# Performance work log

Measured on AMD Instinct MI355X. Metric: run time of the kernel, lower is better.

The kernel has to match this reference:

```python
import jax, jax.numpy as jnp
import numpy as np

B, T, H = 2048, 2048, 32  # batch, sequence steps (columns of input), hidden size


def setup_inputs() -> dict:
    key = jax.random.key(0)
    ks = jax.random.split(key, 5)
    stdv = 1.0 / np.sqrt(H)
    u = lambda k, shp: jax.random.uniform(k, shp, jnp.float32, -stdv, stdv)
    return {
        "x": jax.random.normal(ks[0], (B, T), jnp.float32),
        "weight_ih": u(ks[1], (4 * H, 1)),
        "weight_hh": u(ks[2], (4 * H, H)),
        "bias_ih": u(ks[3], (4 * H,)),
        "bias_hh": u(ks[4], (4 * H,)),
    }


def reference(x, weight_ih, weight_hh, bias_ih, bias_hh):
    Bn, Tn = x.shape
    Hn = weight_hh.shape[1]
    xs = x.T[:, :, None]              # (T, B, 1): step-major inputs
    bias = bias_ih + bias_hh          # (4H,)

    def step(carry, x_t):
        h, c = carry                  # (B, H) each
        gates = x_t @ weight_ih.T + h @ weight_hh.T + bias  # (B, 4H)
        i, f, g, o = jnp.split(gates, 4, axis=1)
        i = jax.nn.sigmoid(i)
        f = jax.nn.sigmoid(f)
        g = jnp.tanh(g)
        o = jax.nn.sigmoid(o)
        # row 0 of the original skips the forget term entirely; with c0 = 0,
        # f * c0 == 0, so this is identical math.
        c_new = f * c + i * g
        h_new = o * jnp.tanh(c_new)
        return (h_new, c_new), h_new

    h0 = jnp.zeros((Bn, Hn), x.dtype)
    c0 = jnp.zeros((Bn, Hn), x.dtype)
    _, ys = jax.lax.scan(step, (h0, c0), xs)   # ys: (T, B, H)
    # torch.cat(h_matrix, 1): step-major blocks of width H along dim 1
    return jnp.transpose(ys, (1, 0, 2)).reshape(Bn, Tn * Hn)
```

## Files before the change

### kernel.cpp

```cpp
#include <hip/hip_runtime.h>
#include <hip/hip_fp16.h>


#define Bsz 2048
#define Tsz 2048
#define Hsz 32

typedef _Float16 v2h __attribute__((ext_vector_type(2)));

__device__ __forceinline__ float fast_rcp(float x) { return __builtin_amdgcn_rcpf(x); }
__device__ __forceinline__ float fast_exp2(float x) { return __builtin_amdgcn_exp2f(x); }

__device__ __forceinline__ float fdot2(uint a, uint b, float c) {
#if __has_builtin(__builtin_amdgcn_fdot2)
    return __builtin_amdgcn_fdot2(__builtin_bit_cast(v2h, a),
                                  __builtin_bit_cast(v2h, b), c, false);
#else
    v2h av = __builtin_bit_cast(v2h, a), bv = __builtin_bit_cast(v2h, b);
    return __fmaf_rn((float)av.x, (float)bv.x,
                     __fmaf_rn((float)av.y, (float)bv.y, c));
#endif
}

__device__ __forceinline__ void plswap(float a, float b, float& r0, float& r1) {
#if __has_builtin(__builtin_amdgcn_permlane32_swap)
    auto r = __builtin_amdgcn_permlane32_swap(__float_as_uint(a), __float_as_uint(b),
                                              false, false);
    r0 = __uint_as_float(r[0]);
    r1 = __uint_as_float(r[1]);
#else
    const bool hi = (threadIdx.x & 32) != 0;
    r0 = hi ? __shfl_xor(b, 32) : a;
    r1 = hi ? b : __shfl_xor(a, 32);
#endif
}

__global__ __launch_bounds__(256, 2) void lstm_fwd_kernel(
    const float* __restrict__ x,
    const float* __restrict__ w_ih,
    const float* __restrict__ w_hh,
    const float* __restrict__ b_ih,
    const float* __restrict__ b_hh,
    float* __restrict__ out)
{
    __shared__ _Float16 hbuf[4][32];
    __shared__ float    xtile[4][2][64];

    const int lane = threadIdx.x & 63;
    const int k    = lane & 31;
    const int gp   = lane >> 5;
    const int wv   = threadIdx.x >> 6;
    const int b    = blockIdx.x * 4 + wv;

    uint WA[16], WB[16];
    {
        const float* rA = w_hh + (size_t)(gp * 64 + k) * 32;
        const float* rB = rA + 32 * 32;
#pragma unroll
        for (int j = 0; j < 16; ++j) {
            WA[j] = __builtin_bit_cast(
                uint, (v2h){(_Float16)rA[2 * j], (_Float16)rA[2 * j + 1]});
            WB[j] = __builtin_bit_cast(
                uint, (v2h){(_Float16)rB[2 * j], (_Float16)rB[2 * j + 1]});
        }
    }
    const int jA = gp * 64 + k, jB = jA + 32;
    const float wiA = w_ih[jA], bsA = b_ih[jA] + b_hh[jA];
    const float wiB = w_ih[jB], bsB = b_ih[jB] + b_hh[jB];

    const float B1 = gp ? -2.885390082f : -1.442695041f;
    const float A1 = gp ? 2.0f : 1.0f;
    const float C1 = gp ? -1.0f : 0.0f;

    float c = 0.0f, h = 0.0f, hprev = 0.0f;
    hbuf[wv][k] = (_Float16)0.0f;

    const float* xrow = x + (size_t)b * Tsz;
    float* op = out + (size_t)b * (size_t)(Tsz * Hsz) + gp * 32 + k;
    const uint4* hl = reinterpret_cast<const uint4*>(&hbuf[wv][0]);

    xtile[wv][0][lane] = xrow[lane];
    float xv = xrow[64 + lane];

#pragma unroll 1
    for (int t0 = 0; t0 < Tsz; t0 += 64) {
        const int cur = (t0 >> 6) & 1;
        xtile[wv][cur ^ 1][lane] = xv;
        int pf = t0 + 128; if (pf >= Tsz) pf = Tsz - 64;
        xv = xrow[pf + lane];
        const float* xl = &xtile[wv][cur][0];

#pragma unroll 1
        for (int tb = 0; tb < 64; tb += 8) {
#pragma unroll
            for (int u = 0; u < 8; ++u) {
                uint4 q0 = hl[0], q1 = hl[1], q2 = hl[2], q3 = hl[3];
                const uint hh[16] = {q0.x, q0.y, q0.z, q0.w,
                                     q1.x, q1.y, q1.z, q1.w,
                                     q2.x, q2.y, q2.z, q2.w,
                                     q3.x, q3.y, q3.z, q3.w};
                const float xt = xl[tb + u];

                float sA0 = 0.f, sA1 = 0.f, sB0 = 0.f, sB1 = 0.f;
#pragma unroll
                for (int j = 0; j < 8; ++j) {
                    sA0 = fdot2(WA[j], hh[j], sA0);
                    sB0 = fdot2(WB[j], hh[j], sB0);
                }
#pragma unroll
                for (int j = 8; j < 16; ++j) {
                    sA1 = fdot2(WA[j], hh[j], sA1);
                    sB1 = fdot2(WB[j], hh[j], sB1);
                }
                const float pA = (sA0 + sA1) + __fmaf_rn(wiA, xt, bsA);
                const float pB = (sB0 + sB1) + __fmaf_rn(wiB, xt, bsB);

                const float a1 = __fmaf_rn(A1, fast_rcp(1.0f + fast_exp2(B1 * pA)), C1);
                const float a2 = fast_rcp(1.0f + fast_exp2(-1.442695041f * pB));

                float i_, g_, f_, o_;
                plswap(a1, a1, i_, g_);
                plswap(a2, a2, f_, o_);

                c = __fmaf_rn(f_, c, i_ * g_);
                const float th =
                    __fmaf_rn(2.0f, fast_rcp(1.0f + fast_exp2(-2.885390082f * c)), -1.0f);
                h = o_ * th;

                hbuf[wv][k] = (_Float16)h;

                if (u & 1) {
                    *op = gp ? h : hprev;
                    op += 64;
                } else {
                    hprev = h;
                }
            }
        }
    }
}

extern "C" void kernel_launch(void* const* d_in, const int* in_sizes, int n_in,
                              void* d_out, int out_size, void* d_ws, size_t ws_size,
                              hipStream_t stream) {
    const float* x    = (const float*)d_in[0];
    const float* w_ih = (const float*)d_in[1];
    const float* w_hh = (const float*)d_in[2];
    const float* b_ih = (const float*)d_in[3];
    const float* b_hh = (const float*)d_in[4];
    float* out = (float*)d_out;

    dim3 grid(Bsz / 4);
    dim3 block(256);
    lstm_fwd_kernel<<<grid, block, 0, stream>>>(x, w_ih, w_hh, b_ih, b_hh, out);
}
```

Before: 606.2 us.

## Broadcast hidden state via readlane and keep x in scalar registers

Replaces the per-step LDS round trip for the recurrent hidden state with 32 v_readlane reads into scalar registers. These are packed into half2 words and fed straight to fdot2. Inputs x are now read per 8-step chunk through wave-uniform loads into registers instead of an LDS tile, helped by marking the wave index uniform with readfirstlane. The aim is to drop LDS write/read latency from the serial dependency chain, at the cost of many readlane and SALU packing ops plus their VALU-to-readlane hazard stalls on each step.

Result: slower. 1.019 ms (+68.2%).

```diff
diff --git a/kernel.cpp b/kernel.cpp
--- a/kernel.cpp
+++ b/kernel.cpp
@@ -11,14 +11,14 @@
 __device__ __forceinline__ float fast_rcp(float x) { return __builtin_amdgcn_rcpf(x); }
 __device__ __forceinline__ float fast_exp2(float x) { return __builtin_amdgcn_exp2f(x); }
 
-__device__ __forceinline__ float fdot2(uint a, uint b, float c) {
+__device__ __forceinline__ float fdot2u(unsigned hs, unsigned wv, float c) {
 #if __has_builtin(__builtin_amdgcn_fdot2)
-    return __builtin_amdgcn_fdot2(__builtin_bit_cast(v2h, a),
-                                  __builtin_bit_cast(v2h, b), c, false);
+    return __builtin_amdgcn_fdot2(__builtin_bit_cast(v2h, hs),
+                                  __builtin_bit_cast(v2h, wv), c, false);
 #else
-    v2h av = __builtin_bit_cast(v2h, a), bv = __builtin_bit_cast(v2h, b);
-    return __fmaf_rn((float)av.x, (float)bv.x,
-                     __fmaf_rn((float)av.y, (float)bv.y, c));
+    v2h a = __builtin_bit_cast(v2h, hs), b = __builtin_bit_cast(v2h, wv);
+    return __fmaf_rn((float)a.x, (float)b.x,
+                     __fmaf_rn((float)a.y, (float)b.y, c));
 #endif
 }
 
@@ -43,25 +43,22 @@
     const float* __restrict__ b_hh,
     float* __restrict__ out)
 {
-    __shared__ _Float16 hbuf[4][32];
-    __shared__ float    xtile[4][2][64];
-
     const int lane = threadIdx.x & 63;
     const int k    = lane & 31;
     const int gp   = lane >> 5;
-    const int wv   = threadIdx.x >> 6;
+    const int wv   = __builtin_amdgcn_readfirstlane((int)(threadIdx.x >> 6));
     const int b    = blockIdx.x * 4 + wv;
 
-    uint WA[16], WB[16];
+    unsigned WA[16], WB[16];
     {
         const float* rA = w_hh + (size_t)(gp * 64 + k) * 32;
         const float* rB = rA + 32 * 32;
 #pragma unroll
         for (int j = 0; j < 16; ++j) {
             WA[j] = __builtin_bit_cast(
-                uint, (v2h){(_Float16)rA[2 * j], (_Float16)rA[2 * j + 1]});
+                unsigned, (v2h){(_Float16)rA[2 * j], (_Float16)rA[2 * j + 1]});
             WB[j] = __builtin_bit_cast(
-                uint, (v2h){(_Float16)rB[2 * j], (_Float16)rB[2 * j + 1]});
+                unsigned, (v2h){(_Float16)rB[2 * j], (_Float16)rB[2 * j + 1]});
         }
     }
     const int jA = gp * 64 + k, jB = jA + 32;
@@ -73,70 +70,68 @@
     const float C1 = gp ? -1.0f : 0.0f;
 
     float c = 0.0f, h = 0.0f, hprev = 0.0f;
-    hbuf[wv][k] = (_Float16)0.0f;
 
     const float* xrow = x + (size_t)b * Tsz;
     float* op = out + (size_t)b * (size_t)(Tsz * Hsz) + gp * 32 + k;
-    const uint4* hl = reinterpret_cast<const uint4*>(&hbuf[wv][0]);
 
-    xtile[wv][0][lane] = xrow[lane];
-    float xv = xrow[64 + lane];
+    float xc[8], xn[8];
+#pragma unroll
+    for (int j = 0; j < 8; ++j) xc[j] = xrow[j];
 
 #pragma unroll 1
-    for (int t0 = 0; t0 < Tsz; t0 += 64) {
-        const int cur = (t0 >> 6) & 1;
-        xtile[wv][cur ^ 1][lane] = xv;
-        int pf = t0 + 128; if (pf >= Tsz) pf = Tsz - 64;
-        xv = xrow[pf + lane];
-        const float* xl = &xtile[wv][cur][0];
+    for (int t0 = 0; t0 < Tsz; t0 += 8) {
+        const int tn = (t0 + 8 < Tsz) ? (t0 + 8) : t0;
+#pragma unroll
+        for (int j = 0; j < 8; ++j) xn[j] = xrow[tn + j];
 
-#pragma unroll 1
-        for (int tb = 0; tb < 64; tb += 8) {
 #pragma unroll
-            for (int u = 0; u < 8; ++u) {
-                uint4 q0 = hl[0], q1 = hl[1], q2 = hl[2], q3 = hl[3];
-                const uint hh[16] = {q0.x, q0.y, q0.z, q0.w,
-                                     q1.x, q1.y, q1.z, q1.w,
-                                     q2.x, q2.y, q2.z, q2.w,
-                                     q3.x, q3.y, q3.z, q3.w};
-                const float xt = xl[tb + u];
+        for (int u = 0; u < 8; ++u) {
+            const unsigned hbits =
+                (unsigned)__builtin_bit_cast(unsigned short, (_Float16)h);
+            unsigned hp[16];
+#pragma unroll
+            for (int m = 0; m < 16; ++m) {
+                unsigned lo = (unsigned)__builtin_amdgcn_readlane((int)hbits, 2 * m);
+                unsigned hi = (unsigned)__builtin_amdgcn_readlane((int)hbits, 2 * m + 1);
+                hp[m] = (lo & 0xffffu) | (hi << 16);
+            }
 
-                float sA0 = 0.f, sA1 = 0.f, sB0 = 0.f, sB1 = 0.f;
+            float sA0 = 0.f, sA1 = 0.f, sB0 = 0.f, sB1 = 0.f;
 #pragma unroll
-                for (int j = 0; j < 8; ++j) {
-                    sA0 = fdot2(WA[j], hh[j], sA0);
-                    sB0 = fdot2(WB[j], hh[j], sB0);
-                }
+            for (int m = 0; m < 8; ++m) {
+                sA0 = fdot2u(hp[m], WA[m], sA0);
+                sB0 = fdot2u(hp[m], WB[m], sB0);
+            }
 #pragma unroll
-                for (int j = 8; j < 16; ++j) {
-                    sA1 = fdot2(WA[j], hh[j], sA1);
-                    sB1 = fdot2(WB[j], hh[j], sB1);
-                }
-                const float pA = (sA0 + sA1) + __fmaf_rn(wiA, xt, bsA);
-                const float pB = (sB0 + sB1) + __fmaf_rn(wiB, xt, bsB);
+            for (int m = 8; m < 16; ++m) {
+                sA1 = fdot2u(hp[m], WA[m], sA1);
+                sB1 = fdot2u(hp[m], WB[m], sB1);
+            }
+            const float xt = xc[u];
+            const float pA = (sA0 + sA1) + __fmaf_rn(wiA, xt, bsA);
+            const float pB = (sB0 + sB1) + __fmaf_rn(wiB, xt, bsB);
 
-                const float a1 = __fmaf_rn(A1, fast_rcp(1.0f + fast_exp2(B1 * pA)), C1);
-                const float a2 = fast_rcp(1.0f + fast_exp2(-1.442695041f * pB));
+            const float a1 = __fmaf_rn(A1, fast_rcp(1.0f + fast_exp2(B1 * pA)), C1);
+            const float a2 = fast_rcp(1.0f + fast_exp2(-1.442695041f * pB));
 
-                float i_, g_, f_, o_;
-                plswap(a1, a1, i_, g_);
-                plswap(a2, a2, f_, o_);
+            float i_, g_, f_, o_;
+            plswap(a1, a1, i_, g_);
+            plswap(a2, a2, f_, o_);
 
-                c = __fmaf_rn(f_, c, i_ * g_);
-                const float th =
-                    __fmaf_rn(2.0f, fast_rcp(1.0f + fast_exp2(-2.885390082f * c)), -1.0f);
-                h = o_ * th;
+            c = __fmaf_rn(f_, c, i_ * g_);
+            const float th =
+                __fmaf_rn(2.0f, fast_rcp(1.0f + fast_exp2(-2.885390082f * c)), -1.0f);
+            h = o_ * th;
 
-                hbuf[wv][k] = (_Float16)h;
-
-                if (u & 1) {
-                    *op = gp ? h : hprev;
-                    op += 64;
-                } else {
-                    hprev = h;
-                }
+            if (u & 1) {
+                *op = gp ? h : hprev;
+                op += 64;
+            } else {
+                hprev = h;
             }
         }
+#pragma unroll
+        for (int j = 0; j < 8; ++j) xc[j] = xn[j];
     }
 }
 
```
